# Performance work log

Hardware: AMD Instinct MI355X
Metric: run time of the kernel (lower is better)

Reference implementation:

```python
import jax, jax.numpy as jnp
import numpy as np

B, T, IN, H, OUT = 2048, 512, 6, 32, 64


def setup_inputs() -> dict:
    key = jax.random.key(0)
    ks = jax.random.split(key, 13)
    s_in = 1.0 / np.sqrt(H)  # torch LSTM/Linear default uniform bound
    u = lambda k, shape, s: jax.random.uniform(k, shape, jnp.float32, -s, s)
    return {
        "imu": jax.random.normal(ks[0], (B, T, IN), jnp.float32),
        # layer 0 (input_size=6)
        "w_ih0": u(ks[1], (4 * H, IN), s_in),
        "w_hh0": u(ks[2], (4 * H, H), s_in),
        "b_ih0": u(ks[3], (4 * H,), s_in),
        "b_hh0": u(ks[4], (4 * H,), s_in),
        # layer 1 (input_size=32)
        "w_ih1": u(ks[5], (4 * H, H), s_in),
        "w_hh1": u(ks[6], (4 * H, H), s_in),
        "b_ih1": u(ks[7], (4 * H,), s_in),
        "b_hh1": u(ks[8], (4 * H,), s_in),
        # heads
        "wf": u(ks[9], (OUT, H), s_in),
        "bf": u(ks[10], (OUT,), s_in),
        "wn": u(ks[11], (OUT, H), s_in),
        "bn": u(ks[12], (OUT,), s_in),
    }


def _lstm_layer(x, w_ih, w_hh, b_ih, b_hh):
    # x: [B, T, in] -> h sequence [B, T, H]; torch gate order: i, f, g, o
    b = x.shape[0]
    # precompute input contribution once: [B, T, 4H]
    gx = jnp.einsum("bti,gi->btg", x, w_ih) + b_ih + b_hh

    def step(carry, g_t):
        h, c = carry
        gates = g_t + h @ w_hh.T  # [B, 4H]
        i = jax.nn.sigmoid(gates[:, :H])
        f = jax.nn.sigmoid(gates[:, H:2 * H])
        g = jnp.tanh(gates[:, 2 * H:3 * H])
        o = jax.nn.sigmoid(gates[:, 3 * H:])
        c = f * c + i * g
        h = o * jnp.tanh(c)
        return (h, c), h

    h0 = jnp.zeros((b, H), x.dtype)
    (_, _), hs = jax.lax.scan(step, (h0, h0), jnp.swapaxes(gx, 0, 1))
    return jnp.swapaxes(hs, 0, 1)  # [B, T, H]


def reference(imu, w_ih0, w_hh0, b_ih0, b_hh0, w_ih1, w_hh1, b_ih1, b_hh1, wf, bf, wn, bn):
    h = _lstm_layer(imu, w_ih0, w_hh0, b_ih0, b_hh0)
    h = _lstm_layer(h, w_ih1, w_hh1, b_ih1, b_hh1)
    last = h[:, -1, :]  # [B, H]
    a_i = last @ wf.T + bf
    R_i = jnp.exp(last @ wn.T + bn)
    return (a_i, R_i)
```

## Files before the change

kernel.cpp:

```cpp
#include <hip/hip_runtime.h>
#include <hip/hip_bf16.h>

#define TT 512
#define BPB 8
#define NBLK (2048 / BPB)
#define OUTD 64

typedef __attribute__((ext_vector_type(8))) short short8;
typedef __attribute__((ext_vector_type(4))) float f32x4;

__device__ __forceinline__ short f2bf(float x) {
    union { float f; unsigned u; } v; v.f = x;
    unsigned r = (v.u + 0x7FFFu + ((v.u >> 16) & 1u)) >> 16;
    return (short)r;
}
__device__ __forceinline__ short cvt_bf16(float x) {
    unsigned r;
    asm("v_cvt_pk_bf16_f32 %0, %1, %1" : "=v"(r) : "v"(x));
    return (short)r;
}
__device__ __forceinline__ float sigm(float x) {
    return __builtin_amdgcn_rcpf(1.f + __expf(-x));
}
__device__ __forceinline__ float tanh_fast(float x) {
    return 2.f * sigm(2.f * x) - 1.f;
}

#define ACT_UPDATE(acc, c, hval)                                   \
    {                                                              \
        float gi = sigm((acc)[0]);                                 \
        float gf = sigm((acc)[1]);                                 \
        float gg = tanh_fast((acc)[2]);                            \
        float go = sigm((acc)[3]);                                 \
        (c) = gf * (c) + gi * gg;                                  \
        (hval) = go * tanh_fast((c));                              \
    }

#define MERGE(mg, a0, a1, colhi)                                   \
    {                                                              \
        _Pragma("unroll")                                          \
        for (int r = 0; r < 4; ++r) {                              \
            float s = __shfl_xor((a1)[r], 8);                      \
            (mg)[r] = (colhi) ? s : (a0)[r];                       \
        }                                                          \
    }

__global__ __launch_bounds__(512, 1) void lstm2_inlane_kernel(
    const float* __restrict__ imu,
    const float* __restrict__ w_ih0, const float* __restrict__ w_hh0,
    const float* __restrict__ b_ih0, const float* __restrict__ b_hh0,
    const float* __restrict__ w_ih1, const float* __restrict__ w_hh1,
    const float* __restrict__ b_ih1, const float* __restrict__ b_hh1,
    const float* __restrict__ wf, const float* __restrict__ bf,
    const float* __restrict__ wn, const float* __restrict__ bn,
    float* __restrict__ out)
{
    const int tid   = threadIdx.x;
    const int l     = tid & 63;
    const int w     = tid >> 6;
    const int layer = w >> 2;
    const int pair  = w & 3;
    const int col   = l & 15;
    const int kg    = l >> 4;
    const bool colhi = (col >= 8);
    const int batch  = col & 7;

    __shared__ __align__(16) short xfrag[TT + 4][8][8];
    __shared__ __align__(16) short h1f[2][16][40];
    __shared__ __align__(16) short h2f[2][16][40];
    __shared__ __align__(16) float lasth[16][36];

    {
        short* p1 = &h1f[0][0][0];
        short* p2 = &h2f[0][0][0];
        for (int i = tid; i < 2 * 16 * 40; i += 512) { p1[i] = 0; p2[i] = 0; }
        short* px = &xfrag[TT][0][0];
        for (int i = tid; i < 4 * 64; i += 512) px[i] = 0;
    }

    {
        const int bg0 = blockIdx.x * BPB;
        for (int p = tid; p < BPB * TT; p += 512) {
            const int b = p >> 9;
            const int t = p & (TT - 1);
            const float* src = imu + ((size_t)(bg0 + b) * TT + t) * 6;
            float2 a0 = *(const float2*)(src);
            float2 a1 = *(const float2*)(src + 2);
            float2 a2 = *(const float2*)(src + 4);
            unsigned* dst = (unsigned*)&xfrag[t][b][0];
            dst[0] = (unsigned short)f2bf(a0.x) | ((unsigned)(unsigned short)f2bf(a0.y) << 16);
            dst[1] = (unsigned short)f2bf(a1.x) | ((unsigned)(unsigned short)f2bf(a1.y) << 16);
            dst[2] = (unsigned short)f2bf(a2.x) | ((unsigned)(unsigned short)f2bf(a2.y) << 16);
            dst[3] = 0u;
        }
    }

    const int t0 = pair * 2, t1 = t0 + 1;
    const int m  = col;
    const int G0 = (m & 3) * 32 + t0 * 4 + (m >> 2);
    const int G1 = (m & 3) * 32 + t1 * 4 + (m >> 2);
    const int u0 = pair * 8 + kg;
    const int u1 = u0 + 4;
    const int myunit = u0 + (colhi ? 4 : 0);

    short8 A00, A01, A10, A11;
    f32x4 bias0, bias1;
    if (layer == 0) {
        #pragma unroll
        for (int j = 0; j < 8; ++j) {
            A00[j] = (kg == 0 && j < 6) ? f2bf(w_ih0[G0 * 6 + j]) : (short)0;
            A10[j] = (kg == 0 && j < 6) ? f2bf(w_ih0[G1 * 6 + j]) : (short)0;
            A01[j] = f2bf(w_hh0[G0 * 32 + kg * 8 + j]);
            A11[j] = f2bf(w_hh0[G1 * 32 + kg * 8 + j]);
        }
        #pragma unroll
        for (int r = 0; r < 4; ++r) {
            bias0[r] = b_ih0[r * 32 + u0] + b_hh0[r * 32 + u0];
            bias1[r] = b_ih0[r * 32 + u1] + b_hh0[r * 32 + u1];
        }
    } else {
        #pragma unroll
        for (int j = 0; j < 8; ++j) {
            A00[j] = f2bf(w_ih1[G0 * 32 + kg * 8 + j]);
            A10[j] = f2bf(w_ih1[G1 * 32 + kg * 8 + j]);
            A01[j] = f2bf(w_hh1[G0 * 32 + kg * 8 + j]);
            A11[j] = f2bf(w_hh1[G1 * 32 + kg * 8 + j]);
        }
        #pragma unroll
        for (int r = 0; r < 4; ++r) {
            bias0[r] = b_ih1[r * 32 + u0] + b_hh1[r * 32 + u0];
            bias1[r] = b_ih1[r * 32 + u1] + b_hh1[r * 32 + u1];
        }
    }

    float c = 0.f;

    const int xb = l & 7;
    const short8* h1r0  = (const short8*)&h1f[0][col][kg * 8];
    const short8* h1r1  = (const short8*)&h1f[1][col][kg * 8];
    const short8* h2r0  = (const short8*)&h2f[0][col][kg * 8];
    const short8* h2r1  = (const short8*)&h2f[1][col][kg * 8];

    __syncthreads();

    short8 xvE = (short8)0, xvO = (short8)0;
    f32x4 xacc0 = bias0, xacc1 = bias1;
    if (layer == 0) {
        short8 xv = *(const short8*)&xfrag[0][xb][0];
        f32x4 a0 = __builtin_amdgcn_mfma_f32_16x16x32_bf16(A00, xv, bias0, 0, 0, 0);
        f32x4 a1 = __builtin_amdgcn_mfma_f32_16x16x32_bf16(A10, xv, bias1, 0, 0, 0);
        f32x4 mg;
        MERGE(mg, a0, a1, colhi);
        float h;
        ACT_UPDATE(mg, c, h);
        h1f[1][batch][myunit] = cvt_bf16(h);
        short8 xv1 = *(const short8*)&xfrag[1][xb][0];
        xacc0 = __builtin_amdgcn_mfma_f32_16x16x32_bf16(A00, xv1, bias0, 0, 0, 0);
        xacc1 = __builtin_amdgcn_mfma_f32_16x16x32_bf16(A10, xv1, bias1, 0, 0, 0);
        xvE = *(const short8*)&xfrag[2][xb][0];
    }
    __syncthreads();

#define STEP(T, H1R, H2R, WP, XVC, XVL)                                         \
    {                                                                           \
        if (layer == 0) {                                                       \
            short8 hv = *(H1R);                                                 \
            f32x4 a0 = __builtin_amdgcn_mfma_f32_16x16x32_bf16(A01, hv, xacc0, 0, 0, 0); \
            f32x4 a1 = __builtin_amdgcn_mfma_f32_16x16x32_bf16(A11, hv, xacc1, 0, 0, 0); \
            f32x4 mg;                                                           \
            MERGE(mg, a0, a1, colhi);                                           \
            float h;                                                            \
            ACT_UPDATE(mg, c, h);                                               \
            h1f[WP][batch][myunit] = cvt_bf16(h);                               \
            xacc0 = __builtin_amdgcn_mfma_f32_16x16x32_bf16(A00, XVC, bias0, 0, 0, 0); \
            xacc1 = __builtin_amdgcn_mfma_f32_16x16x32_bf16(A10, XVC, bias1, 0, 0, 0); \
            XVL = *(const short8*)&xfrag[(T) + 3][xb][0];                       \
        } else {                                                                \
            short8 av = *(H1R);                                                 \
            short8 bv = *(H2R);                                                 \
            f32x4 a0 = __builtin_amdgcn_mfma_f32_16x16x32_bf16(A00, av, bias0, 0, 0, 0); \
            f32x4 a1 = __builtin_amdgcn_mfma_f32_16x16x32_bf16(A10, av, bias1, 0, 0, 0); \
            a0 = __builtin_amdgcn_mfma_f32_16x16x32_bf16(A01, bv, a0, 0, 0, 0); \
            a1 = __builtin_amdgcn_mfma_f32_16x16x32_bf16(A11, bv, a1, 0, 0, 0); \
            f32x4 mg;                                                           \
            MERGE(mg, a0, a1, colhi);                                           \
            float h;                                                            \
            ACT_UPDATE(mg, c, h);                                               \
            h2f[WP][batch][myunit] = cvt_bf16(h);                               \
        }                                                                       \
        __syncthreads();                                                        \
    }

    #pragma unroll 1
    for (int t = 0; t < TT - 2; t += 2) {
        STEP(t,     h1r1, h2r1, 0, xvE, xvO)
        STEP(t + 1, h1r0, h2r0, 1, xvO, xvE)
    }
    STEP(TT - 2, h1r1, h2r1, 0, xvE, xvO)

    if (layer == 1) {
        short8 av = *h1r0;
        short8 bv = *h2r0;
        f32x4 a0 = __builtin_amdgcn_mfma_f32_16x16x32_bf16(A00, av, bias0, 0, 0, 0);
        f32x4 a1 = __builtin_amdgcn_mfma_f32_16x16x32_bf16(A10, av, bias1, 0, 0, 0);
        a0 = __builtin_amdgcn_mfma_f32_16x16x32_bf16(A01, bv, a0, 0, 0, 0);
        a1 = __builtin_amdgcn_mfma_f32_16x16x32_bf16(A11, bv, a1, 0, 0, 0);
        f32x4 mg;
        MERGE(mg, a0, a1, colhi);
        float h;
        ACT_UPDATE(mg, c, h);
        lasth[batch][myunit] = h;
    }
    __syncthreads();

    {
        const int b = tid >> 6;
        const int o = tid & 63;
        float accF = bf[o], accN = bn[o];
        const float4* wf4 = (const float4*)(wf + o * 32);
        const float4* wn4 = (const float4*)(wn + o * 32);
        const float4* hv4 = (const float4*)&lasth[b][0];
        #pragma unroll
        for (int k = 0; k < 8; ++k) {
            float4 h4 = hv4[k];
            float4 f4 = wf4[k];
            float4 n4 = wn4[k];
            accF += f4.x * h4.x + f4.y * h4.y + f4.z * h4.z + f4.w * h4.w;
            accN += n4.x * h4.x + n4.y * h4.y + n4.z * h4.z + n4.w * h4.w;
        }
        const size_t bg = (size_t)blockIdx.x * BPB + b;
        out[bg * OUTD + o] = accF;
        out[(size_t)2048 * OUTD + bg * OUTD + o] = __expf(accN);
    }
}

extern "C" void kernel_launch(void* const* d_in, const int* in_sizes, int n_in,
                              void* d_out, int out_size, void* d_ws, size_t ws_size,
                              hipStream_t stream) {
    const float* imu   = (const float*)d_in[0];
    const float* w_ih0 = (const float*)d_in[1];
    const float* w_hh0 = (const float*)d_in[2];
    const float* b_ih0 = (const float*)d_in[3];
    const float* b_hh0 = (const float*)d_in[4];
    const float* w_ih1 = (const float*)d_in[5];
    const float* w_hh1 = (const float*)d_in[6];
    const float* b_ih1 = (const float*)d_in[7];
    const float* b_hh1 = (const float*)d_in[8];
    const float* wf    = (const float*)d_in[9];
    const float* bf    = (const float*)d_in[10];
    const float* wn    = (const float*)d_in[11];
    const float* bn    = (const float*)d_in[12];
    float* out = (float*)d_out;

    lstm2_inlane_kernel<<<dim3(NBLK), dim3(512), 0, stream>>>(
        imu, w_ih0, w_hh0, b_ih0, b_hh0,
        w_ih1, w_hh1, b_ih1, b_hh1,
        wf, bf, wn, bn, out);
}
```

Before: 173.9 us.

## Halve batch per block and fold four MFMA tiles per wave

Each block now handles 4 batch rows instead of 8 with 256 threads (2 waves per layer), and the launch bounds allow two blocks per CU. Each wave issues four MFMAs per step and folds them with a two-level shuffle, so each lane owns one unit for one batch. The grid doubles to 512 blocks so more CUs are busy at once, and the per-step barrier now spans 4 waves instead of 8. In exchange each wave does twice the MFMA and shuffle work per step on the serial recurrence path and holds more weight registers.

```diff
diff --git a/kernel.cpp b/kernel.cpp
--- a/kernel.cpp
+++ b/kernel.cpp
@@ -2,7 +2,7 @@
 #include <hip/hip_bf16.h>
 
 #define TT 512
-#define BPB 8
+#define BPB 4
 #define NBLK (2048 / BPB)
 #define OUTD 64
 
@@ -36,16 +36,20 @@
         (hval) = go * tanh_fast((c));                              \
     }
 
-#define MERGE(mg, a0, a1, colhi)                                   \
+#define FOLD4(mg, a0, a1, a2, a3, c4, c8)                          \
     {                                                              \
         _Pragma("unroll")                                          \
         for (int r = 0; r < 4; ++r) {                              \
-            float s = __shfl_xor((a1)[r], 8);                      \
-            (mg)[r] = (colhi) ? s : (a0)[r];                       \
+            float s1 = __shfl_xor((a1)[r], 4);                     \
+            float m1 = (c4) ? s1 : (a0)[r];                        \
+            float s2 = __shfl_xor((a3)[r], 4);                     \
+            float m2 = (c4) ? s2 : (a2)[r];                        \
+            float s3 = __shfl_xor(m2, 8);                          \
+            (mg)[r] = (c8) ? s3 : m1;                              \
         }                                                          \
     }
 
-__global__ __launch_bounds__(512, 1) void lstm2_inlane_kernel(
+__global__ __launch_bounds__(256, 2) void lstm2_fold4_kernel(
     const float* __restrict__ imu,
     const float* __restrict__ w_ih0, const float* __restrict__ w_hh0,
     const float* __restrict__ b_ih0, const float* __restrict__ b_hh0,
@@ -58,36 +62,39 @@
     const int tid   = threadIdx.x;
     const int l     = tid & 63;
     const int w     = tid >> 6;
-    const int layer = w >> 2;
-    const int pair  = w & 3;
-    const int col   = l & 15;
-    const int kg    = l >> 4;
-    const bool colhi = (col >= 8);
-    const int batch  = col & 7;
-
-    __shared__ __align__(16) short xfrag[TT + 4][8][8];
+    const int layer = w >> 1;
+    const int p     = w & 1;
+    const int c     = l & 15;
+    const int q     = l >> 4;
+    const int b     = c & 3;
+    const int tsel  = c >> 2;
+    const bool c4   = (c & 4) != 0;
+    const bool c8   = (c & 8) != 0;
+    const int unit  = 16 * p + 4 * tsel + q;
+
+    __shared__ __align__(16) short xfrag[TT + 4][BPB][8];
     __shared__ __align__(16) short h1f[2][16][40];
     __shared__ __align__(16) short h2f[2][16][40];
-    __shared__ __align__(16) float lasth[16][36];
+    __shared__ __align__(16) float lasth[BPB][36];
 
     {
         short* p1 = &h1f[0][0][0];
         short* p2 = &h2f[0][0][0];
-        for (int i = tid; i < 2 * 16 * 40; i += 512) { p1[i] = 0; p2[i] = 0; }
+        for (int i = tid; i < 2 * 16 * 40; i += 256) { p1[i] = 0; p2[i] = 0; }
         short* px = &xfrag[TT][0][0];
-        for (int i = tid; i < 4 * 64; i += 512) px[i] = 0;
+        for (int i = tid; i < 4 * BPB * 8; i += 256) px[i] = 0;
     }
 
     {
         const int bg0 = blockIdx.x * BPB;
-        for (int p = tid; p < BPB * TT; p += 512) {
-            const int b = p >> 9;
-            const int t = p & (TT - 1);
-            const float* src = imu + ((size_t)(bg0 + b) * TT + t) * 6;
+        for (int pp = tid; pp < BPB * TT; pp += 256) {
+            const int bb = pp >> 9;
+            const int t  = pp & (TT - 1);
+            const float* src = imu + ((size_t)(bg0 + bb) * TT + t) * 6;
             float2 a0 = *(const float2*)(src);
             float2 a1 = *(const float2*)(src + 2);
             float2 a2 = *(const float2*)(src + 4);
-            unsigned* dst = (unsigned*)&xfrag[t][b][0];
+            unsigned* dst = (unsigned*)&xfrag[t][bb][0];
             dst[0] = (unsigned short)f2bf(a0.x) | ((unsigned)(unsigned short)f2bf(a0.y) << 16);
             dst[1] = (unsigned short)f2bf(a1.x) | ((unsigned)(unsigned short)f2bf(a1.y) << 16);
             dst[2] = (unsigned short)f2bf(a2.x) | ((unsigned)(unsigned short)f2bf(a2.y) << 16);
@@ -95,69 +102,63 @@
         }
     }
 
-    const int t0 = pair * 2, t1 = t0 + 1;
-    const int m  = col;
-    const int G0 = (m & 3) * 32 + t0 * 4 + (m >> 2);
-    const int G1 = (m & 3) * 32 + t1 * 4 + (m >> 2);
-    const int u0 = pair * 8 + kg;
-    const int u1 = u0 + 4;
-    const int myunit = u0 + (colhi ? 4 : 0);
-
-    short8 A00, A01, A10, A11;
-    f32x4 bias0, bias1;
+    short8 AF[4], AS[4];
+    f32x4 bias[4];
+    #pragma unroll
+    for (int tp = 0; tp < 4; ++tp) {
+        const int tau = 4 * p + tp;
+        const int G   = (c & 3) * 32 + tau * 4 + (c >> 2);
+        const int u   = 16 * p + 4 * tp + q;
+        if (layer == 0) {
+            #pragma unroll
+            for (int j = 0; j < 8; ++j) {
+                AF[tp][j] = (q == 0 && j < 6) ? f2bf(w_ih0[G * 6 + j]) : (short)0;
+                AS[tp][j] = f2bf(w_hh0[G * 32 + q * 8 + j]);
+            }
+            #pragma unroll
+            for (int r = 0; r < 4; ++r)
+                bias[tp][r] = b_ih0[r * 32 + u] + b_hh0[r * 32 + u];
+        } else {
+            #pragma unroll
+            for (int j = 0; j < 8; ++j) {
+                AF[tp][j] = f2bf(w_ih1[G * 32 + q * 8 + j]);
+                AS[tp][j] = f2bf(w_hh1[G * 32 + q * 8 + j]);
+            }
+            #pragma unroll
+            for (int r = 0; r < 4; ++r)
+                bias[tp][r] = b_ih1[r * 32 + u] + b_hh1[r * 32 + u];
+        }
+    }
+
+    float cst = 0.f;
+
+    const short8* h1r0 = (const short8*)&h1f[0][c][q * 8];
+    const short8* h1r1 = (const short8*)&h1f[1][c][q * 8];
+    const short8* h2r0 = (const short8*)&h2f[0][c][q * 8];
+    const short8* h2r1 = (const short8*)&h2f[1][c][q * 8];
+
+    __syncthreads();
+
+    short8 xvE = (short8)0, xvO = (short8)0;
+    f32x4 xacc[4];
+    #pragma unroll
+    for (int tp = 0; tp < 4; ++tp) xacc[tp] = bias[tp];
     if (layer == 0) {
+        short8 xv = *(const short8*)&xfrag[0][b][0];
+        f32x4 a0 = __builtin_amdgcn_mfma_f32_16x16x32_bf16(AF[0], xv, bias[0], 0, 0, 0);
+        f32x4 a1 = __builtin_amdgcn_mfma_f32_16x16x32_bf16(AF[1], xv, bias[1], 0, 0, 0);
+        f32x4 a2 = __builtin_amdgcn_mfma_f32_16x16x32_bf16(AF[2], xv, bias[2], 0, 0, 0);
+        f32x4 a3 = __builtin_amdgcn_mfma_f32_16x16x32_bf16(AF[3], xv, bias[3], 0, 0, 0);
+        f32x4 mg;
+        FOLD4(mg, a0, a1, a2, a3, c4, c8);
+        float h;
+        ACT_UPDATE(mg, cst, h);
+        h1f[1][b][unit] = cvt_bf16(h);
+        short8 xv1 = *(const short8*)&xfrag[1][b][0];
         #pragma unroll
-        for (int j = 0; j < 8; ++j) {
-            A00[j] = (kg == 0 && j < 6) ? f2bf(w_ih0[G0 * 6 + j]) : (short)0;
-            A10[j] = (kg == 0 && j < 6) ? f2bf(w_ih0[G1 * 6 + j]) : (short)0;
-            A01[j] = f2bf(w_hh0[G0 * 32 + kg * 8 + j]);
-            A11[j] = f2bf(w_hh0[G1 * 32 + kg * 8 + j]);
-        }
-        #pragma unroll
-        for (int r = 0; r < 4; ++r) {
-            bias0[r] = b_ih0[r * 32 + u0] + b_hh0[r * 32 + u0];
-            bias1[r] = b_ih0[r * 32 + u1] + b_hh0[r * 32 + u1];
-        }
-    } else {
-        #pragma unroll
-        for (int j = 0; j < 8; ++j) {
-            A00[j] = f2bf(w_ih1[G0 * 32 + kg * 8 + j]);
-            A10[j] = f2bf(w_ih1[G1 * 32 + kg * 8 + j]);
-            A01[j] = f2bf(w_hh1[G0 * 32 + kg * 8 + j]);
-            A11[j] = f2bf(w_hh1[G1 * 32 + kg * 8 + j]);
-        }
-        #pragma unroll
-        for (int r = 0; r < 4; ++r) {
-            bias0[r] = b_ih1[r * 32 + u0] + b_hh1[r * 32 + u0];
-            bias1[r] = b_ih1[r * 32 + u1] + b_hh1[r * 32 + u1];
-        }
-    }
-
-    float c = 0.f;
-
-    const int xb = l & 7;
-    const short8* h1r0  = (const short8*)&h1f[0][col][kg * 8];
-    const short8* h1r1  = (const short8*)&h1f[1][col][kg * 8];
-    const short8* h2r0  = (const short8*)&h2f[0][col][kg * 8];
-    const short8* h2r1  = (const short8*)&h2f[1][col][kg * 8];
-
-    __syncthreads();
-
-    short8 xvE = (short8)0, xvO = (short8)0;
-    f32x4 xacc0 = bias0, xacc1 = bias1;
-    if (layer == 0) {
-        short8 xv = *(const short8*)&xfrag[0][xb][0];
-        f32x4 a0 = __builtin_amdgcn_mfma_f32_16x16x32_bf16(A00, xv, bias0, 0, 0, 0);
-        f32x4 a1 = __builtin_amdgcn_mfma_f32_16x16x32_bf16(A10, xv, bias1, 0, 0, 0);
-        f32x4 mg;
-        MERGE(mg, a0, a1, colhi);
-        float h;
-        ACT_UPDATE(mg, c, h);
-        h1f[1][batch][myunit] = cvt_bf16(h);
-        short8 xv1 = *(const short8*)&xfrag[1][xb][0];
-        xacc0 = __builtin_amdgcn_mfma_f32_16x16x32_bf16(A00, xv1, bias0, 0, 0, 0);
-        xacc1 = __builtin_amdgcn_mfma_f32_16x16x32_bf16(A10, xv1, bias1, 0, 0, 0);
-        xvE = *(const short8*)&xfrag[2][xb][0];
+        for (int tp = 0; tp < 4; ++tp)
+            xacc[tp] = __builtin_amdgcn_mfma_f32_16x16x32_bf16(AF[tp], xv1, bias[tp], 0, 0, 0);
+        xvE = *(const short8*)&xfrag[2][b][0];
     }
     __syncthreads();
 
@@ -165,28 +166,35 @@
     {                                                                           \
         if (layer == 0) {                                                       \
             short8 hv = *(H1R);                                                 \
-            f32x4 a0 = __builtin_amdgcn_mfma_f32_16x16x32_bf16(A01, hv, xacc0, 0, 0, 0); \
-            f32x4 a1 = __builtin_amdgcn_mfma_f32_16x16x32_bf16(A11, hv, xacc1, 0, 0, 0); \
+            f32x4 a0 = __builtin_amdgcn_mfma_f32_16x16x32_bf16(AS[0], hv, xacc[0], 0, 0, 0); \
+            f32x4 a1 = __builtin_amdgcn_mfma_f32_16x16x32_bf16(AS[1], hv, xacc[1], 0, 0, 0); \
+            f32x4 a2 = __builtin_amdgcn_mfma_f32_16x16x32_bf16(AS[2], hv, xacc[2], 0, 0, 0); \
+            f32x4 a3 = __builtin_amdgcn_mfma_f32_16x16x32_bf16(AS[3], hv, xacc[3], 0, 0, 0); \
             f32x4 mg;                                                           \
-            MERGE(mg, a0, a1, colhi);                                           \
+            FOLD4(mg, a0, a1, a2, a3, c4, c8);                                  \
             float h;                                                            \
-            ACT_UPDATE(mg, c, h);                                               \
-            h1f[WP][batch][myunit] = cvt_bf16(h);                               \
-            xacc0 = __builtin_amdgcn_mfma_f32_16x16x32_bf16(A00, XVC, bias0, 0, 0, 0); \
-            xacc1 = __builtin_amdgcn_mfma_f32_16x16x32_bf16(A10, XVC, bias1, 0, 0, 0); \
-            XVL = *(const short8*)&xfrag[(T) + 3][xb][0];                       \
+            ACT_UPDATE(mg, cst, h);                                             \
+            h1f[WP][b][unit] = cvt_bf16(h);                                     \
+            _Pragma("unroll")                                                   \
+            for (int tp = 0; tp < 4; ++tp)                                      \
+                xacc[tp] = __builtin_amdgcn_mfma_f32_16x16x32_bf16(AF[tp], XVC, bias[tp], 0, 0, 0); \
+            XVL = *(const short8*)&xfrag[(T) + 3][b][0];                        \
         } else {                                                                \
             short8 av = *(H1R);                                                 \
             short8 bv = *(H2R);                                                 \
-            f32x4 a0 = __builtin_amdgcn_mfma_f32_16x16x32_bf16(A00, av, bias0, 0, 0, 0); \
-            f32x4 a1 = __builtin_amdgcn_mfma_f32_16x16x32_bf16(A10, av, bias1, 0, 0, 0); \
-            a0 = __builtin_amdgcn_mfma_f32_16x16x32_bf16(A01, bv, a0, 0, 0, 0); \
-            a1 = __builtin_amdgcn_mfma_f32_16x16x32_bf16(A11, bv, a1, 0, 0, 0); \
+            f32x4 a0 = __builtin_amdgcn_mfma_f32_16x16x32_bf16(AF[0], av, bias[0], 0, 0, 0); \
+            f32x4 a1 = __builtin_amdgcn_mfma_f32_16x16x32_bf16(AF[1], av, bias[1], 0, 0, 0); \
+            f32x4 a2 = __builtin_amdgcn_mfma_f32_16x16x32_bf16(AF[2], av, bias[2], 0, 0, 0); \
+            f32x4 a3 = __builtin_amdgcn_mfma_f32_16x16x32_bf16(AF[3], av, bias[3], 0, 0, 0); \
+            a0 = __builtin_amdgcn_mfma_f32_16x16x32_bf16(AS[0], bv, a0, 0, 0, 0); \
+            a1 = __builtin_amdgcn_mfma_f32_16x16x32_bf16(AS[1], bv, a1, 0, 0, 0); \
+            a2 = __builtin_amdgcn_mfma_f32_16x16x32_bf16(AS[2], bv, a2, 0, 0, 0); \
+            a3 = __builtin_amdgcn_mfma_f32_16x16x32_bf16(AS[3], bv, a3, 0, 0, 0); \
             f32x4 mg;                                                           \
-            MERGE(mg, a0, a1, colhi);                                           \
+            FOLD4(mg, a0, a1, a2, a3, c4, c8);                                  \
             float h;                                                            \
-            ACT_UPDATE(mg, c, h);                                               \
-            h2f[WP][batch][myunit] = cvt_bf16(h);                               \
+            ACT_UPDATE(mg, cst, h);                                             \
+            h2f[WP][b][unit] = cvt_bf16(h);                                     \
         }                                                                       \
         __syncthreads();                                                        \
     }
@@ -201,25 +209,29 @@
     if (layer == 1) {
         short8 av = *h1r0;
         short8 bv = *h2r0;
-        f32x4 a0 = __builtin_amdgcn_mfma_f32_16x16x32_bf16(A00, av, bias0, 0, 0, 0);
-        f32x4 a1 = __builtin_amdgcn_mfma_f32_16x16x32_bf16(A10, av, bias1, 0, 0, 0);
-        a0 = __builtin_amdgcn_mfma_f32_16x16x32_bf16(A01, bv, a0, 0, 0, 0);
-        a1 = __builtin_amdgcn_mfma_f32_16x16x32_bf16(A11, bv, a1, 0, 0, 0);
+        f32x4 a0 = __builtin_amdgcn_mfma_f32_16x16x32_bf16(AF[0], av, bias[0], 0, 0, 0);
+        f32x4 a1 = __builtin_amdgcn_mfma_f32_16x16x32_bf16(AF[1], av, bias[1], 0, 0, 0);
+        f32x4 a2 = __builtin_amdgcn_mfma_f32_16x16x32_bf16(AF[2], av, bias[2], 0, 0, 0);
+        f32x4 a3 = __builtin_amdgcn_mfma_f32_16x16x32_bf16(AF[3], av, bias[3], 0, 0, 0);
+        a0 = __builtin_amdgcn_mfma_f32_16x16x32_bf16(AS[0], bv, a0, 0, 0, 0);
+        a1 = __builtin_amdgcn_mfma_f32_16x16x32_bf16(AS[1], bv, a1, 0, 0, 0);
+        a2 = __builtin_amdgcn_mfma_f32_16x16x32_bf16(AS[2], bv, a2, 0, 0, 0);
+        a3 = __builtin_amdgcn_mfma_f32_16x16x32_bf16(AS[3], bv, a3, 0, 0, 0);
         f32x4 mg;
-        MERGE(mg, a0, a1, colhi);
+        FOLD4(mg, a0, a1, a2, a3, c4, c8);
         float h;
-        ACT_UPDATE(mg, c, h);
-        lasth[batch][myunit] = h;
+        ACT_UPDATE(mg, cst, h);
+        lasth[b][unit] = h;
     }
     __syncthreads();
 
     {
-        const int b = tid >> 6;
-        const int o = tid & 63;
+        const int bb = tid >> 6;
+        const int o  = tid & 63;
         float accF = bf[o], accN = bn[o];
         const float4* wf4 = (const float4*)(wf + o * 32);
         const float4* wn4 = (const float4*)(wn + o * 32);
-        const float4* hv4 = (const float4*)&lasth[b][0];
+        const float4* hv4 = (const float4*)&lasth[bb][0];
         #pragma unroll
         for (int k = 0; k < 8; ++k) {
             float4 h4 = hv4[k];
@@ -228,7 +240,7 @@
             accF += f4.x * h4.x + f4.y * h4.y + f4.z * h4.z + f4.w * h4.w;
             accN += n4.x * h4.x + n4.y * h4.y + n4.z * h4.z + n4.w * h4.w;
         }
-        const size_t bg = (size_t)blockIdx.x * BPB + b;
+        const size_t bg = (size_t)blockIdx.x * BPB + bb;
         out[bg * OUTD + o] = accF;
         out[(size_t)2048 * OUTD + bg * OUTD + o] = __expf(accN);
     }
@@ -252,7 +264,7 @@
     const float* bn    = (const float*)d_in[12];
     float* out = (float*)d_out;
 
-    lstm2_inlane_kernel<<<dim3(NBLK), dim3(512), 0, stream>>>(
+    lstm2_fold4_kernel<<<dim3(NBLK), dim3(256), 0, stream>>>(
         imu, w_ih0, w_hh0, b_ih0, b_hh0,
         w_ih1, w_hh1, b_ih1, b_hh1,
         wf, bf, wn, bn, out);
```

After: 241.7 us. 1.39x slower.

## Process two independent 8-batch groups per block to halve grid and interleave chains

Applied to the files above, without the earlier changes.

Each block now handles 16 batch rows as two independent 8-row groups, doubling the MFMA and activation work per wave between barriers and halving the number of blocks to 128. The two recurrence chains are interleaved so their MFMA and transcendental latencies can overlap, and each barrier now covers twice as much work. The cost is more registers and shared memory per block, and fewer blocks than the device has compute units, which leaves some of them idle.

```diff
diff --git a/kernel.cpp b/kernel.cpp
--- a/kernel.cpp
+++ b/kernel.cpp
@@ -2,7 +2,7 @@
 #include <hip/hip_bf16.h>
 
 #define TT 512
-#define BPB 8
+#define BPB 16
 #define NBLK (2048 / BPB)
 #define OUTD 64
 
@@ -45,7 +45,7 @@
         }                                                          \
     }
 
-__global__ __launch_bounds__(512, 1) void lstm2_inlane_kernel(
+__global__ __launch_bounds__(512, 1) void lstm2_dual_kernel(
     const float* __restrict__ imu,
     const float* __restrict__ w_ih0, const float* __restrict__ w_hh0,
     const float* __restrict__ b_ih0, const float* __restrict__ b_hh0,
@@ -65,29 +65,29 @@
     const bool colhi = (col >= 8);
     const int batch  = col & 7;
 
-    __shared__ __align__(16) short xfrag[TT + 4][8][8];
-    __shared__ __align__(16) short h1f[2][16][40];
-    __shared__ __align__(16) short h2f[2][16][40];
+    __shared__ __align__(16) short xfrag[TT + 4][BPB][8];
+    __shared__ __align__(16) short h1f[2][2][16][40];
+    __shared__ __align__(16) short h2f[2][2][16][40];
     __shared__ __align__(16) float lasth[16][36];
 
     {
-        short* p1 = &h1f[0][0][0];
-        short* p2 = &h2f[0][0][0];
-        for (int i = tid; i < 2 * 16 * 40; i += 512) { p1[i] = 0; p2[i] = 0; }
+        short* p1 = &h1f[0][0][0][0];
+        short* p2 = &h2f[0][0][0][0];
+        for (int i = tid; i < 2 * 2 * 16 * 40; i += 512) { p1[i] = 0; p2[i] = 0; }
         short* px = &xfrag[TT][0][0];
-        for (int i = tid; i < 4 * 64; i += 512) px[i] = 0;
+        if (tid < 4 * BPB * 8) px[tid] = 0;
     }
 
     {
         const int bg0 = blockIdx.x * BPB;
         for (int p = tid; p < BPB * TT; p += 512) {
-            const int b = p >> 9;
-            const int t = p & (TT - 1);
-            const float* src = imu + ((size_t)(bg0 + b) * TT + t) * 6;
+            const int bb = p >> 9;
+            const int t  = p & (TT - 1);
+            const float* src = imu + ((size_t)(bg0 + bb) * TT + t) * 6;
             float2 a0 = *(const float2*)(src);
             float2 a1 = *(const float2*)(src + 2);
             float2 a2 = *(const float2*)(src + 4);
-            unsigned* dst = (unsigned*)&xfrag[t][b][0];
+            unsigned* dst = (unsigned*)&xfrag[t][bb][0];
             dst[0] = (unsigned short)f2bf(a0.x) | ((unsigned)(unsigned short)f2bf(a0.y) << 16);
             dst[1] = (unsigned short)f2bf(a1.x) | ((unsigned)(unsigned short)f2bf(a1.y) << 16);
             dst[2] = (unsigned short)f2bf(a2.x) | ((unsigned)(unsigned short)f2bf(a2.y) << 16);
@@ -133,93 +133,138 @@
         }
     }
 
-    float c = 0.f;
-
-    const int xb = l & 7;
-    const short8* h1r0  = (const short8*)&h1f[0][col][kg * 8];
-    const short8* h1r1  = (const short8*)&h1f[1][col][kg * 8];
-    const short8* h2r0  = (const short8*)&h2f[0][col][kg * 8];
-    const short8* h2r1  = (const short8*)&h2f[1][col][kg * 8];
+    float cA = 0.f, cB = 0.f;
+
+    const int xbA = l & 7;
+    const int xbB = (l & 7) + 8;
+    const short8* h1A0 = (const short8*)&h1f[0][0][col][kg * 8];
+    const short8* h1A1 = (const short8*)&h1f[0][1][col][kg * 8];
+    const short8* h1B0 = (const short8*)&h1f[1][0][col][kg * 8];
+    const short8* h1B1 = (const short8*)&h1f[1][1][col][kg * 8];
+    const short8* h2A0 = (const short8*)&h2f[0][0][col][kg * 8];
+    const short8* h2A1 = (const short8*)&h2f[0][1][col][kg * 8];
+    const short8* h2B0 = (const short8*)&h2f[1][0][col][kg * 8];
+    const short8* h2B1 = (const short8*)&h2f[1][1][col][kg * 8];
 
     __syncthreads();
 
-    short8 xvE = (short8)0, xvO = (short8)0;
-    f32x4 xacc0 = bias0, xacc1 = bias1;
+    short8 xvEA = (short8)0, xvOA = (short8)0;
+    short8 xvEB = (short8)0, xvOB = (short8)0;
+    f32x4 xaccA0 = bias0, xaccA1 = bias1, xaccB0 = bias0, xaccB1 = bias1;
     if (layer == 0) {
-        short8 xv = *(const short8*)&xfrag[0][xb][0];
-        f32x4 a0 = __builtin_amdgcn_mfma_f32_16x16x32_bf16(A00, xv, bias0, 0, 0, 0);
-        f32x4 a1 = __builtin_amdgcn_mfma_f32_16x16x32_bf16(A10, xv, bias1, 0, 0, 0);
-        f32x4 mg;
-        MERGE(mg, a0, a1, colhi);
-        float h;
-        ACT_UPDATE(mg, c, h);
-        h1f[1][batch][myunit] = cvt_bf16(h);
-        short8 xv1 = *(const short8*)&xfrag[1][xb][0];
-        xacc0 = __builtin_amdgcn_mfma_f32_16x16x32_bf16(A00, xv1, bias0, 0, 0, 0);
-        xacc1 = __builtin_amdgcn_mfma_f32_16x16x32_bf16(A10, xv1, bias1, 0, 0, 0);
-        xvE = *(const short8*)&xfrag[2][xb][0];
+        short8 xvA = *(const short8*)&xfrag[0][xbA][0];
+        short8 xvB = *(const short8*)&xfrag[0][xbB][0];
+        f32x4 aA0 = __builtin_amdgcn_mfma_f32_16x16x32_bf16(A00, xvA, bias0, 0, 0, 0);
+        f32x4 aA1 = __builtin_amdgcn_mfma_f32_16x16x32_bf16(A10, xvA, bias1, 0, 0, 0);
+        f32x4 aB0 = __builtin_amdgcn_mfma_f32_16x16x32_bf16(A00, xvB, bias0, 0, 0, 0);
+        f32x4 aB1 = __builtin_amdgcn_mfma_f32_16x16x32_bf16(A10, xvB, bias1, 0, 0, 0);
+        f32x4 mgA, mgB;
+        MERGE(mgA, aA0, aA1, colhi);
+        MERGE(mgB, aB0, aB1, colhi);
+        float hA, hB;
+        ACT_UPDATE(mgA, cA, hA);
+        ACT_UPDATE(mgB, cB, hB);
+        h1f[0][1][batch][myunit] = cvt_bf16(hA);
+        h1f[1][1][batch][myunit] = cvt_bf16(hB);
+        short8 x1A = *(const short8*)&xfrag[1][xbA][0];
+        short8 x1B = *(const short8*)&xfrag[1][xbB][0];
+        xaccA0 = __builtin_amdgcn_mfma_f32_16x16x32_bf16(A00, x1A, bias0, 0, 0, 0);
+        xaccA1 = __builtin_amdgcn_mfma_f32_16x16x32_bf16(A10, x1A, bias1, 0, 0, 0);
+        xaccB0 = __builtin_amdgcn_mfma_f32_16x16x32_bf16(A00, x1B, bias0, 0, 0, 0);
+        xaccB1 = __builtin_amdgcn_mfma_f32_16x16x32_bf16(A10, x1B, bias1, 0, 0, 0);
+        xvEA = *(const short8*)&xfrag[2][xbA][0];
+        xvEB = *(const short8*)&xfrag[2][xbB][0];
     }
     __syncthreads();
 
-#define STEP(T, H1R, H2R, WP, XVC, XVL)                                         \
+#define STEP(T, H1RA, H1RB, H2RA, H2RB, WP, XVCA, XVLA, XVCB, XVLB)             \
     {                                                                           \
         if (layer == 0) {                                                       \
-            short8 hv = *(H1R);                                                 \
-            f32x4 a0 = __builtin_amdgcn_mfma_f32_16x16x32_bf16(A01, hv, xacc0, 0, 0, 0); \
-            f32x4 a1 = __builtin_amdgcn_mfma_f32_16x16x32_bf16(A11, hv, xacc1, 0, 0, 0); \
-            f32x4 mg;                                                           \
-            MERGE(mg, a0, a1, colhi);                                           \
-            float h;                                                            \
-            ACT_UPDATE(mg, c, h);                                               \
-            h1f[WP][batch][myunit] = cvt_bf16(h);                               \
-            xacc0 = __builtin_amdgcn_mfma_f32_16x16x32_bf16(A00, XVC, bias0, 0, 0, 0); \
-            xacc1 = __builtin_amdgcn_mfma_f32_16x16x32_bf16(A10, XVC, bias1, 0, 0, 0); \
-            XVL = *(const short8*)&xfrag[(T) + 3][xb][0];                       \
+            short8 hvA = *(H1RA);                                               \
+            short8 hvB = *(H1RB);                                               \
+            f32x4 aA0 = __builtin_amdgcn_mfma_f32_16x16x32_bf16(A01, hvA, xaccA0, 0, 0, 0); \
+            f32x4 aA1 = __builtin_amdgcn_mfma_f32_16x16x32_bf16(A11, hvA, xaccA1, 0, 0, 0); \
+            f32x4 aB0 = __builtin_amdgcn_mfma_f32_16x16x32_bf16(A01, hvB, xaccB0, 0, 0, 0); \
+            f32x4 aB1 = __builtin_amdgcn_mfma_f32_16x16x32_bf16(A11, hvB, xaccB1, 0, 0, 0); \
+            f32x4 mgA, mgB;                                                     \
+            MERGE(mgA, aA0, aA1, colhi);                                        \
+            MERGE(mgB, aB0, aB1, colhi);                                        \
+            float hA, hB;                                                       \
+            ACT_UPDATE(mgA, cA, hA);                                            \
+            ACT_UPDATE(mgB, cB, hB);                                            \
+            h1f[0][WP][batch][myunit] = cvt_bf16(hA);                           \
+            h1f[1][WP][batch][myunit] = cvt_bf16(hB);                           \
+            xaccA0 = __builtin_amdgcn_mfma_f32_16x16x32_bf16(A00, XVCA, bias0, 0, 0, 0); \
+            xaccA1 = __builtin_amdgcn_mfma_f32_16x16x32_bf16(A10, XVCA, bias1, 0, 0, 0); \
+            xaccB0 = __builtin_amdgcn_mfma_f32_16x16x32_bf16(A00, XVCB, bias0, 0, 0, 0); \
+            xaccB1 = __builtin_amdgcn_mfma_f32_16x16x32_bf16(A10, XVCB, bias1, 0, 0, 0); \
+            XVLA = *(const short8*)&xfrag[(T) + 3][xbA][0];                     \
+            XVLB = *(const short8*)&xfrag[(T) + 3][xbB][0];                     \
         } else {                                                                \
-            short8 av = *(H1R);                                                 \
-            short8 bv = *(H2R);                                                 \
-            f32x4 a0 = __builtin_amdgcn_mfma_f32_16x16x32_bf16(A00, av, bias0, 0, 0, 0); \
-            f32x4 a1 = __builtin_amdgcn_mfma_f32_16x16x32_bf16(A10, av, bias1, 0, 0, 0); \
-            a0 = __builtin_amdgcn_mfma_f32_16x16x32_bf16(A01, bv, a0, 0, 0, 0); \
-            a1 = __builtin_amdgcn_mfma_f32_16x16x32_bf16(A11, bv, a1, 0, 0, 0); \
-            f32x4 mg;                                                           \
-            MERGE(mg, a0, a1, colhi);                                           \
-            float h;                                                            \
-            ACT_UPDATE(mg, c, h);                                               \
-            h2f[WP][batch][myunit] = cvt_bf16(h);                               \
+            short8 avA = *(H1RA);                                               \
+            short8 avB = *(H1RB);                                               \
+            short8 bvA = *(H2RA);                                               \
+            short8 bvB = *(H2RB);                                               \
+            f32x4 aA0 = __builtin_amdgcn_mfma_f32_16x16x32_bf16(A00, avA, bias0, 0, 0, 0); \
+            f32x4 aA1 = __builtin_amdgcn_mfma_f32_16x16x32_bf16(A10, avA, bias1, 0, 0, 0); \
+            f32x4 aB0 = __builtin_amdgcn_mfma_f32_16x16x32_bf16(A00, avB, bias0, 0, 0, 0); \
+            f32x4 aB1 = __builtin_amdgcn_mfma_f32_16x16x32_bf16(A10, avB, bias1, 0, 0, 0); \
+            aA0 = __builtin_amdgcn_mfma_f32_16x16x32_bf16(A01, bvA, aA0, 0, 0, 0); \
+            aA1 = __builtin_amdgcn_mfma_f32_16x16x32_bf16(A11, bvA, aA1, 0, 0, 0); \
+            aB0 = __builtin_amdgcn_mfma_f32_16x16x32_bf16(A01, bvB, aB0, 0, 0, 0); \
+            aB1 = __builtin_amdgcn_mfma_f32_16x16x32_bf16(A11, bvB, aB1, 0, 0, 0); \
+            f32x4 mgA, mgB;                                                     \
+            MERGE(mgA, aA0, aA1, colhi);                                        \
+            MERGE(mgB, aB0, aB1, colhi);                                        \
+            float hA, hB;                                                       \
+            ACT_UPDATE(mgA, cA, hA);                                            \
+            ACT_UPDATE(mgB, cB, hB);                                            \
+            h2f[0][WP][batch][myunit] = cvt_bf16(hA);                           \
+            h2f[1][WP][batch][myunit] = cvt_bf16(hB);                           \
         }                                                                       \
         __syncthreads();                                                        \
     }
 
     #pragma unroll 1
     for (int t = 0; t < TT - 2; t += 2) {
-        STEP(t,     h1r1, h2r1, 0, xvE, xvO)
-        STEP(t + 1, h1r0, h2r0, 1, xvO, xvE)
-    }
-    STEP(TT - 2, h1r1, h2r1, 0, xvE, xvO)
+        STEP(t,     h1A1, h1B1, h2A1, h2B1, 0, xvEA, xvOA, xvEB, xvOB)
+        STEP(t + 1, h1A0, h1B0, h2A0, h2B0, 1, xvOA, xvEA, xvOB, xvEB)
+    }
+    STEP(TT - 2, h1A1, h1B1, h2A1, h2B1, 0, xvEA, xvOA, xvEB, xvOB)
 
     if (layer == 1) {
-        short8 av = *h1r0;
-        short8 bv = *h2r0;
-        f32x4 a0 = __builtin_amdgcn_mfma_f32_16x16x32_bf16(A00, av, bias0, 0, 0, 0);
-        f32x4 a1 = __builtin_amdgcn_mfma_f32_16x16x32_bf16(A10, av, bias1, 0, 0, 0);
-        a0 = __builtin_amdgcn_mfma_f32_16x16x32_bf16(A01, bv, a0, 0, 0, 0);
-        a1 = __builtin_amdgcn_mfma_f32_16x16x32_bf16(A11, bv, a1, 0, 0, 0);
-        f32x4 mg;
-        MERGE(mg, a0, a1, colhi);
-        float h;
-        ACT_UPDATE(mg, c, h);
-        lasth[batch][myunit] = h;
+        short8 avA = *h1A0;
+        short8 avB = *h1B0;
+        short8 bvA = *h2A0;
+        short8 bvB = *h2B0;
+        f32x4 aA0 = __builtin_amdgcn_mfma_f32_16x16x32_bf16(A00, avA, bias0, 0, 0, 0);
+        f32x4 aA1 = __builtin_amdgcn_mfma_f32_16x16x32_bf16(A10, avA, bias1, 0, 0, 0);
+        f32x4 aB0 = __builtin_amdgcn_mfma_f32_16x16x32_bf16(A00, avB, bias0, 0, 0, 0);
+        f32x4 aB1 = __builtin_amdgcn_mfma_f32_16x16x32_bf16(A10, avB, bias1, 0, 0, 0);
+        aA0 = __builtin_amdgcn_mfma_f32_16x16x32_bf16(A01, bvA, aA0, 0, 0, 0);
+        aA1 = __builtin_amdgcn_mfma_f32_16x16x32_bf16(A11, bvA, aA1, 0, 0, 0);
+        aB0 = __builtin_amdgcn_mfma_f32_16x16x32_bf16(A01, bvB, aB0, 0, 0, 0);
+        aB1 = __builtin_amdgcn_mfma_f32_16x16x32_bf16(A11, bvB, aB1, 0, 0, 0);
+        f32x4 mgA, mgB;
+        MERGE(mgA, aA0, aA1, colhi);
+        MERGE(mgB, aB0, aB1, colhi);
+        float hA, hB;
+        ACT_UPDATE(mgA, cA, hA);
+        ACT_UPDATE(mgB, cB, hB);
+        lasth[batch][myunit] = hA;
+        lasth[batch + 8][myunit] = hB;
     }
     __syncthreads();
 
-    {
-        const int b = tid >> 6;
-        const int o = tid & 63;
+    #pragma unroll
+    for (int rep = 0; rep < 2; ++rep) {
+        const int idx = tid + rep * 512;
+        const int bb  = idx >> 6;
+        const int o   = idx & 63;
         float accF = bf[o], accN = bn[o];
         const float4* wf4 = (const float4*)(wf + o * 32);
         const float4* wn4 = (const float4*)(wn + o * 32);
-        const float4* hv4 = (const float4*)&lasth[b][0];
+        const float4* hv4 = (const float4*)&lasth[bb][0];
         #pragma unroll
         for (int k = 0; k < 8; ++k) {
             float4 h4 = hv4[k];
@@ -228,7 +273,7 @@
             accF += f4.x * h4.x + f4.y * h4.y + f4.z * h4.z + f4.w * h4.w;
             accN += n4.x * h4.x + n4.y * h4.y + n4.z * h4.z + n4.w * h4.w;
         }
-        const size_t bg = (size_t)blockIdx.x * BPB + b;
+        const size_t bg = (size_t)blockIdx.x * BPB + bb;
         out[bg * OUTD + o] = accF;
         out[(size_t)2048 * OUTD + bg * OUTD + o] = __expf(accN);
     }
@@ -252,7 +297,7 @@
     const float* bn    = (const float*)d_in[12];
     float* out = (float*)d_out;
 
-    lstm2_inlane_kernel<<<dim3(NBLK), dim3(512), 0, stream>>>(
+    lstm2_dual_kernel<<<dim3(NBLK), dim3(512), 0, stream>>>(
         imu, w_ih0, w_hh0, b_ih0, b_hh0,
         w_ih1, w_hh1, b_ih1, b_hh1,
         wf, bf, wn, bn, out);
```

Result: slower. 302.1 us (+73.8%).
